# Kernel tuning notes

Hardware: AMD Instinct MI355X
Metric: run time of the kernel (lower is better)

The kernel has to match this reference:

```python
import jax, jax.numpy as jnp
import numpy as np

B, N, D, H = 4, 8192, 1024, 16
HD = D // H  # head dim 64
EPS = 1e-5


def setup_inputs() -> dict:
    key = jax.random.key(0)
    ks = jax.random.split(key, 12)
    s = 1.0 / np.sqrt(D)
    return {
        "query": jax.random.normal(ks[0], (B, N, D), jnp.float32),
        "Wq": jax.random.normal(ks[1], (D, D), jnp.float32) * s,
        "bq": jax.random.normal(ks[2], (D,), jnp.float32) * 0.01,
        "Wk": jax.random.normal(ks[3], (D, D), jnp.float32) * s,
        "bk": jax.random.normal(ks[4], (D,), jnp.float32) * 0.01,
        "Wv": jax.random.normal(ks[5], (D, D), jnp.float32) * s,
        "bv": jax.random.normal(ks[6], (D,), jnp.float32) * 0.01,
        "Wu": jax.random.normal(ks[7], (D, D), jnp.float32) * s,
        "bu": jax.random.normal(ks[8], (D,), jnp.float32) * 0.01,
        "Wo": jax.random.normal(ks[9], (D, D), jnp.float32) * s,
        "bo": jax.random.normal(ks[10], (D,), jnp.float32) * 0.01,
        "ln_w": jnp.ones((D,), jnp.float32),
        "ln_b": jnp.zeros((D,), jnp.float32),
    }


def _abs_clamp(t, min_mag=0.01, max_mag=100.0):
    return jnp.clip(jnp.abs(t), min_mag, max_mag) * jnp.sign(t)


def _heads(x):  # [b, n, h*d] -> [b, h, n, d]
    b, n, _ = x.shape
    return x.reshape(b, n, H, HD).transpose(0, 2, 1, 3)


def reference(query, Wq, bq, Wk, bk, Wv, bv, Wu, bu, Wo, bo, ln_w, ln_b):
    q = jax.nn.relu(_heads(query @ Wq + bq))  # [b,h,n,d]
    k = jax.nn.relu(_heads(query @ Wk + bk))
    v = _heads(query @ Wv + bv)
    u = query @ Wu + bu  # [b,n,D]
    # global linear-attention reduction: kv[b,h,d,e] = sum_n k v
    kv = jnp.einsum('bhnd,bhne->bhde', k, v)
    kv = _abs_clamp(kv)
    out = jnp.einsum('bhnd,bhde->bhne', q, kv)  # [b,h,n,d]
    out = out.transpose(0, 2, 1, 3).reshape(query.shape)  # [b,n,D]
    # LayerNorm over last dim
    mu = jnp.mean(out, axis=-1, keepdims=True)
    var = jnp.var(out, axis=-1, keepdims=True)
    out = (out - mu) * jax.lax.rsqrt(var + EPS) * ln_w + ln_b
    out = u * out
    return out @ Wo + bo
```

## Files before the change

kernel.cpp:

```cpp
#include <hip/hip_runtime.h>

#define M_TOT 32768

typedef float f32x4 __attribute__((ext_vector_type(4)));
typedef short s16x8 __attribute__((ext_vector_type(8)));

#define AS1(p) ((__attribute__((address_space(1))) void*)(p))
#define AS3(p) ((__attribute__((address_space(3))) void*)(p))

#define BARRIER() asm volatile("s_barrier" ::: "memory")
#define VMCNT4() asm volatile("s_waitcnt vmcnt(4)" ::: "memory")
#define VMCNT2() asm volatile("s_waitcnt vmcnt(2)" ::: "memory")
#define VMCNT0() asm volatile("s_waitcnt vmcnt(0)" ::: "memory")

__device__ __forceinline__ short f2bf(float f) {
    unsigned u = __builtin_bit_cast(unsigned, f);
    u += 0x7fffu + ((u >> 16) & 1u);
    return (short)(u >> 16);
}
__device__ __forceinline__ float bf2f(short s) {
    unsigned u = ((unsigned)(unsigned short)s) << 16;
    return __builtin_bit_cast(float, u);
}

__global__ void conv_x(const float* __restrict__ x, short* __restrict__ y) {
    const size_t nchunk = (size_t)M_TOT * 1024 / 8;
    const size_t stride = (size_t)gridDim.x * blockDim.x;
    for (size_t c = (size_t)blockIdx.x * blockDim.x + threadIdx.x; c < nchunk; c += stride) {
        const float4* src = (const float4*)(x + c * 8);
        float4 a = src[0], b = src[1];
        s16x8 r;
        r[0] = f2bf(a.x); r[1] = f2bf(a.y); r[2] = f2bf(a.z); r[3] = f2bf(a.w);
        r[4] = f2bf(b.x); r[5] = f2bf(b.y); r[6] = f2bf(b.z); r[7] = f2bf(b.w);
        *(s16x8*)(y + c * 8) = r;
    }
}

__global__ void conv_w(const float* __restrict__ Wq, const float* __restrict__ Wk,
                       const float* __restrict__ Wv, const float* __restrict__ Wu,
                       const float* __restrict__ Wo, short* __restrict__ Wcat) {
    const int c = blockIdx.x * 256 + threadIdx.x;
    const int np = c >> 8;
    const int k0 = (c & 255) << 2;
    const float* W = (np < 1024) ? Wq : (np < 2048) ? Wk : (np < 3072) ? Wv
                   : (np < 4096) ? Wu : Wo;
    const int n = np & 1023;
    short4 r;
    r.x = f2bf(W[(size_t)(k0 + 0) * 1024 + n]);
    r.y = f2bf(W[(size_t)(k0 + 1) * 1024 + n]);
    r.z = f2bf(W[(size_t)(k0 + 2) * 1024 + n]);
    r.w = f2bf(W[(size_t)(k0 + 3) * 1024 + n]);
    *(short4*)(Wcat + (size_t)np * 1024 + k0) = r;
}

__global__ void conv_bias(const float* __restrict__ bq, const float* __restrict__ bk,
                          const float* __restrict__ bv, const float* __restrict__ bu,
                          const float* __restrict__ bo, float* __restrict__ bcat) {
    const int i = blockIdx.x * 256 + threadIdx.x;
    const float* b = (i < 1024) ? bq : (i < 2048) ? bk : (i < 3072) ? bv
                   : (i < 4096) ? bu : bo;
    bcat[i] = b[i & 1023];
}

template <int MODE>
__global__ __launch_bounds__(512, 2) void gemm8(
        const short* __restrict__ A, const short* __restrict__ W,
        const float* __restrict__ bias,
        short* __restrict__ qb, short* __restrict__ ktb,
        short* __restrict__ vtb, short* __restrict__ ub,
        float* __restrict__ outb) {
    extern __shared__ char lds[];
    const int tid = threadIdx.x;
    const int wave = tid >> 6, lane = tid & 63;
    const int r16 = lane & 15, g = lane >> 4;
    const int moff = (wave >> 2) << 7;
    const int noff = (wave & 3) << 6;

    const int nwg = (MODE == 0) ? 2048 : 512;
    const int NB = (MODE == 0) ? 16 : 4;
    const int bid = blockIdx.x;
    const int swz = (bid & 7) * (nwg >> 3) + (bid >> 3);
    const int mblk = swz / NB, nblk = swz % NB;
    const int row0 = mblk << 8, col0 = nblk << 8;

    const int rswz = r16 & 7;
    const int ck0 = (g ^ rswz) << 4;
    const int ck1 = ((4 + g) ^ rswz) << 4;
    const int rowbA = (moff + r16) << 7;
    const int rowbB = (noff + r16) << 7;

    const char* baseA = (const char*)A + (size_t)(row0 + wave * 8 + (lane >> 3)) * 2048
                        + (((lane & 7) ^ ((lane >> 3) & 7)) << 4);
    const char* baseB = (const char*)W + (size_t)(col0 + wave * 8 + (lane >> 3)) * 2048
                        + (((lane & 7) ^ ((lane >> 3) & 7)) << 4);

#define STG(BASE, J, T, DST)                                                   \
    __builtin_amdgcn_global_load_lds(                                          \
        AS1((BASE) + (size_t)(J) * 131072 + (size_t)(T) * 128),                \
        AS3((DST) + (J) * 8192 + wave * 1024), 16, 0, 0)

#define RDA(V, M, BUFA) {                                                      \
    (V)[0] = *(const s16x8*)((BUFA) + rowbA + (M) * 2048 + ck0);               \
    (V)[1] = *(const s16x8*)((BUFA) + rowbA + (M) * 2048 + ck1); }

#define RDB(V, N, BUFB) {                                                      \
    (V)[0] = *(const s16x8*)((BUFB) + rowbB + (N) * 2048 + ck0);               \
    (V)[1] = *(const s16x8*)((BUFB) + rowbB + (N) * 2048 + ck1); }

#define MF16(P)                                                                \
    _Pragma("unroll") for (int kk = 0; kk < 2; ++kk)                           \
        _Pragma("unroll") for (int n = 0; n < 4; ++n) {                        \
            acc[2*(P)][n]   = __builtin_amdgcn_mfma_f32_16x16x32_bf16(afr[0][kk], bfr[n][kk], acc[2*(P)][n], 0, 0, 0);   \
            acc[2*(P)+1][n] = __builtin_amdgcn_mfma_f32_16x16x32_bf16(afr[1][kk], bfr[n][kk], acc[2*(P)+1][n], 0, 0, 0); \
        }

#define TILE(T, DOSTAGE, TR2, TR4) {                                           \
    char* bA_ = lds + ((T) & 1) * 65536; char* bB_ = bA_ + 32768;              \
    char* sA_ = lds + (((T) + 1) & 1) * 65536; char* sB_ = sA_ + 32768;        \
    s16x8 afr[2][2];                                                           \
    if (DOSTAGE) { STG(baseB, 0, (T) + 1, sB_); STG(baseB, 1, (T) + 1, sB_); } \
    _Pragma("unroll") for (int n = 0; n < 4; ++n) RDB(bfr[n], n, bB_);         \
    RDA(afr[0], 0, bA_); RDA(afr[1], 1, bA_);                                  \
    BARRIER(); __builtin_amdgcn_s_setprio(1); MF16(0);                         \
    __builtin_amdgcn_s_setprio(0); BARRIER();                                  \
    if (DOSTAGE) { STG(baseB, 2, (T) + 1, sB_); STG(baseB, 3, (T) + 1, sB_); } \
    RDA(afr[0], 2, bA_); RDA(afr[1], 3, bA_);                                  \
    BARRIER(); __builtin_amdgcn_s_setprio(1); MF16(1);                         \
    __builtin_amdgcn_s_setprio(0); TR2; BARRIER();                             \
    if (DOSTAGE) { STG(baseA, 0, (T) + 1, sA_); STG(baseA, 2, (T) + 1, sA_); } \
    RDA(afr[0], 4, bA_); RDA(afr[1], 5, bA_);                                  \
    BARRIER(); __builtin_amdgcn_s_setprio(1); MF16(2);                         \
    __builtin_amdgcn_s_setprio(0); BARRIER();                                  \
    if (DOSTAGE) { STG(baseA, 1, (T) + 1, sA_); STG(baseA, 3, (T) + 1, sA_); } \
    RDA(afr[0], 6, bA_); RDA(afr[1], 7, bA_);                                  \
    BARRIER(); __builtin_amdgcn_s_setprio(1); MF16(3);                         \
    __builtin_amdgcn_s_setprio(0); TR4; BARRIER();                             \
}

    f32x4 acc[8][4] = {};
    s16x8 bfr[4][2];

    STG(baseB, 0, 0, lds + 32768); STG(baseB, 1, 0, lds + 32768);
    STG(baseB, 2, 0, lds + 32768); STG(baseB, 3, 0, lds + 32768);
    STG(baseA, 0, 0, lds);         STG(baseA, 2, 0, lds);
    STG(baseA, 1, 0, lds);         STG(baseA, 3, 0, lds);
    VMCNT2();
    BARRIER();

    #pragma unroll 1
    for (int t = 0; t < 15; ++t) TILE(t, true, VMCNT4(), VMCNT2());
    TILE(15, false, VMCNT0(), (void)0);

    const int rj = (lane >> 4) << 2;
    if (MODE == 1) {
        #pragma unroll
        for (int n = 0; n < 4; ++n) {
            const int gn = col0 + noff + n * 16 + r16;
            const float bv = bias[gn];
            #pragma unroll
            for (int m = 0; m < 8; ++m) {
                const int gm0 = row0 + moff + m * 16 + rj;
                #pragma unroll
                for (int j = 0; j < 4; ++j)
                    outb[(size_t)(gm0 + j) * 1024 + gn] = acc[m][n][j] + bv;
            }
        }
    } else {
        const int seg = col0 >> 10;
        if (seg == 0 || seg == 3) {
            short* dst = (seg == 0) ? qb : ub;
            const bool do_relu = (seg == 0);
            #pragma unroll
            for (int n = 0; n < 4; ++n) {
                const int gn = col0 + noff + n * 16 + r16;
                const int f = gn & 1023;
                const float bv = bias[gn];
                #pragma unroll
                for (int m = 0; m < 8; ++m) {
                    const int gm0 = row0 + moff + m * 16 + rj;
                    #pragma unroll
                    for (int j = 0; j < 4; ++j) {
                        float val = acc[m][n][j] + bv;
                        if (do_relu) val = fmaxf(val, 0.0f);
                        dst[(size_t)(gm0 + j) * 1024 + f] = f2bf(val);
                    }
                }
            }
        } else {
            short* dst = (seg == 1) ? ktb : vtb;
            const bool do_relu = (seg == 1);
            #pragma unroll
            for (int n = 0; n < 4; ++n) {
                const int gn = col0 + noff + n * 16 + r16;
                const int hd = gn & 1023;
                const float bv = bias[gn];
                #pragma unroll
                for (int m = 0; m < 8; ++m) {
                    const int gm0 = row0 + moff + m * 16 + rj;
                    const int b = gm0 >> 13;
                    const int ntok = gm0 & 8191;
                    float v0 = acc[m][n][0] + bv, v1 = acc[m][n][1] + bv;
                    float v2 = acc[m][n][2] + bv, v3 = acc[m][n][3] + bv;
                    if (do_relu) {
                        v0 = fmaxf(v0, 0.0f); v1 = fmaxf(v1, 0.0f);
                        v2 = fmaxf(v2, 0.0f); v3 = fmaxf(v3, 0.0f);
                    }
                    short4 pk;
                    pk.x = f2bf(v0); pk.y = f2bf(v1); pk.z = f2bf(v2); pk.w = f2bf(v3);
                    *(short4*)(dst + ((size_t)(b * 1024 + hd)) * 8192 + ntok) = pk;
                }
            }
        }
    }
#undef TILE
#undef MF16
#undef RDB
#undef RDA
#undef STG
}

__global__ __launch_bounds__(256) void kv_partial(const short* __restrict__ ktb,
                                                  const short* __restrict__ vtb,
                                                  float* __restrict__ kvp) {
    __shared__ float red[4][4096];
    const int slice = blockIdx.x;
    const int bh = blockIdx.y;
    const int wave = threadIdx.x >> 6, lane = threadIdx.x & 63;
    const int r16 = lane & 15;
    const short* kb = ktb + (size_t)bh * 64 * 8192;
    const short* vb = vtb + (size_t)bh * 64 * 8192;
    const int n0 = (slice << 10) + (wave << 8);
    f32x4 acc[4][4] = {};
    for (int s = 0; s < 8; ++s) {
        const int nk = n0 + (s << 5) + ((lane >> 4) << 3);
        s16x8 af[4], bf[4];
        #pragma unroll
        for (int m = 0; m < 4; ++m) af[m] = *(const s16x8*)(kb + (size_t)(m * 16 + r16) * 8192 + nk);
        #pragma unroll
        for (int n = 0; n < 4; ++n) bf[n] = *(const s16x8*)(vb + (size_t)(n * 16 + r16) * 8192 + nk);
        #pragma unroll
        for (int m = 0; m < 4; ++m)
            #pragma unroll
            for (int n = 0; n < 4; ++n)
                acc[m][n] = __builtin_amdgcn_mfma_f32_16x16x32_bf16(af[m], bf[n], acc[m][n], 0, 0, 0);
    }
    const int rj = (lane >> 4) << 2;
    #pragma unroll
    for (int m = 0; m < 4; ++m)
        #pragma unroll
        for (int n = 0; n < 4; ++n)
            #pragma unroll
            for (int j = 0; j < 4; ++j)
                red[wave][(m * 16 + rj + j) * 64 + n * 16 + r16] = acc[m][n][j];
    __syncthreads();
    float* dst = kvp + ((size_t)slice * 64 + bh) * 4096;
    const int i0 = threadIdx.x * 16;
    #pragma unroll
    for (int e = 0; e < 16; e += 4) {
        f32x4 a0 = *(const f32x4*)&red[0][i0 + e];
        f32x4 a1 = *(const f32x4*)&red[1][i0 + e];
        f32x4 a2 = *(const f32x4*)&red[2][i0 + e];
        f32x4 a3 = *(const f32x4*)&red[3][i0 + e];
        *(f32x4*)&dst[i0 + e] = (a0 + a1) + (a2 + a3);
    }
}

__global__ void kv_reduce(const float* __restrict__ kvp, short* __restrict__ kvt) {
    const int bh = blockIdx.x;
    for (int i = threadIdx.x; i < 4096; i += 256) {
        float s = 0.0f;
        #pragma unroll
        for (int sl = 0; sl < 8; ++sl)
            s += kvp[((size_t)sl * 64 + bh) * 4096 + i];
        float a = fabsf(s);
        float cmag = fminf(fmaxf(a, 0.01f), 100.0f);
        float r = (s > 0.0f) ? cmag : ((s < 0.0f) ? -cmag : 0.0f);
        const int d = i >> 6, e = i & 63;
        kvt[(size_t)bh * 4096 + e * 64 + d] = f2bf(r);
    }
}

__global__ __launch_bounds__(256) void qkv_ln(const short* __restrict__ qb,
                                              const short* __restrict__ kvt,
                                              const short* __restrict__ ub,
                                              const float* __restrict__ lnw,
                                              const float* __restrict__ lnb,
                                              short* __restrict__ yb) {
    __shared__ short tr[4][1024];
    const int wave = threadIdx.x >> 6, lane = threadIdx.x & 63;
    const int r16 = lane & 15, g = lane >> 4;
    const size_t rowB = (size_t)blockIdx.x * 64 + wave * 16;
    const int bh0 = (int)((rowB >> 13) << 4);
    const short* qrow = qb + (rowB + r16) * 1024 + g * 8;

    float s[4] = {0, 0, 0, 0}, sq[4] = {0, 0, 0, 0};
    for (int h = 0; h < 16; ++h) {
        const short* kvb = kvt + (size_t)(bh0 + h) * 4096 + g * 8;
        f32x4 a4[4] = {};
        #pragma unroll
        for (int kk = 0; kk < 2; ++kk) {
            const s16x8 af = *(const s16x8*)(qrow + h * 64 + kk * 32);
            #pragma unroll
            for (int n = 0; n < 4; ++n) {
                const s16x8 bf = *(const s16x8*)(kvb + (n * 16 + r16) * 64 + kk * 32);
                a4[n] = __builtin_amdgcn_mfma_f32_16x16x32_bf16(af, bf, a4[n], 0, 0, 0);
            }
        }
        #pragma unroll
        for (int n = 0; n < 4; ++n)
            #pragma unroll
            for (int j = 0; j < 4; ++j) {
                const float v = a4[n][j];
                s[j] += v; sq[j] += v * v;
            }
    }
    #pragma unroll
    for (int j = 0; j < 4; ++j) {
        #pragma unroll
        for (int mk = 1; mk < 16; mk <<= 1) {
            s[j] += __shfl_xor(s[j], mk);
            sq[j] += __shfl_xor(sq[j], mk);
        }
    }
    float mu[4], rs[4];
    #pragma unroll
    for (int j = 0; j < 4; ++j) {
        mu[j] = s[j] * (1.0f / 1024.0f);
        const float var = sq[j] * (1.0f / 1024.0f) - mu[j] * mu[j];
        rs[j] = rsqrtf(var + 1e-5f);
    }

    short* trw = &tr[wave][0];
    const int rdr = lane >> 3;
    const int c0 = (lane & 7) * 8;
    for (int h = 0; h < 16; ++h) {
        const short* kvb = kvt + (size_t)(bh0 + h) * 4096 + g * 8;
        f32x4 a4[4] = {};
        #pragma unroll
        for (int kk = 0; kk < 2; ++kk) {
            const s16x8 af = *(const s16x8*)(qrow + h * 64 + kk * 32);
            #pragma unroll
            for (int n = 0; n < 4; ++n) {
                const s16x8 bf = *(const s16x8*)(kvb + (n * 16 + r16) * 64 + kk * 32);
                a4[n] = __builtin_amdgcn_mfma_f32_16x16x32_bf16(af, bf, a4[n], 0, 0, 0);
            }
        }
        #pragma unroll
        for (int n = 0; n < 4; ++n) {
            const float lw = lnw[h * 64 + n * 16 + r16];
            const float lb = lnb[h * 64 + n * 16 + r16];
            #pragma unroll
            for (int j = 0; j < 4; ++j) {
                const float val = (a4[n][j] - mu[j]) * rs[j] * lw + lb;
                trw[(g * 4 + j) * 64 + ((n ^ g) * 16 + r16)] = f2bf(val);
            }
        }
        #pragma unroll
        for (int p = 0; p < 2; ++p) {
            const int r = rdr + p * 8;
            const s16x8 t = *(const s16x8*)&trw[r * 64 + (((c0 >> 4) ^ (r >> 2)) * 16) + (c0 & 15)];
            const s16x8 uu = *(const s16x8*)(ub + (rowB + r) * 1024 + h * 64 + c0);
            s16x8 o;
            #pragma unroll
            for (int e = 0; e < 8; ++e)
                o[e] = f2bf(bf2f(t[e]) * bf2f(uu[e]));
            *(s16x8*)(yb + (rowB + r) * 1024 + h * 64 + c0) = o;
        }
    }
}

extern "C" void kernel_launch(void* const* d_in, const int* in_sizes, int n_in,
                              void* d_out, int out_size, void* d_ws, size_t ws_size,
                              hipStream_t stream) {
    (void)in_sizes; (void)n_in; (void)out_size;
    const float* query = (const float*)d_in[0];
    const float* Wq = (const float*)d_in[1];
    const float* bq = (const float*)d_in[2];
    const float* Wk = (const float*)d_in[3];
    const float* bk = (const float*)d_in[4];
    const float* Wv = (const float*)d_in[5];
    const float* bv = (const float*)d_in[6];
    const float* Wu = (const float*)d_in[7];
    const float* bu = (const float*)d_in[8];
    const float* Wo = (const float*)d_in[9];
    const float* bo = (const float*)d_in[10];
    const float* lnw = (const float*)d_in[11];
    const float* lnb = (const float*)d_in[12];
    float* out = (float*)d_out;
    char* ws = (char*)d_ws;
    if (ws_size < 380129280u) return;

    short* Xb   = (short*)(ws);
    short* Wcat = (short*)(ws + 67108864);
    float* bcat = (float*)(ws + 77594624);
    short* qb   = (short*)(ws + 77615104);
    short* ktb  = (short*)(ws + 144723968);
    short* vtb  = (short*)(ws + 211832832);
    short* ub   = (short*)(ws + 278941696);
    float* kvp  = (float*)(ws + 346050560);
    short* kvt  = (short*)(ws + 379604992);
    short* yb   = Xb;

    hipFuncSetAttribute(reinterpret_cast<const void*>(&gemm8<0>),
                        hipFuncAttributeMaxDynamicSharedMemorySize, 131072);
    hipFuncSetAttribute(reinterpret_cast<const void*>(&gemm8<1>),
                        hipFuncAttributeMaxDynamicSharedMemorySize, 131072);

    conv_x<<<2048, 256, 0, stream>>>(query, Xb);
    conv_w<<<5120, 256, 0, stream>>>(Wq, Wk, Wv, Wu, Wo, Wcat);
    conv_bias<<<20, 256, 0, stream>>>(bq, bk, bv, bu, bo, bcat);
    gemm8<0><<<2048, 512, 131072, stream>>>(Xb, Wcat, bcat, qb, ktb, vtb, ub, nullptr);
    kv_partial<<<dim3(8, 64), 256, 0, stream>>>(ktb, vtb, kvp);
    kv_reduce<<<64, 256, 0, stream>>>(kvp, kvt);
    qkv_ln<<<512, 256, 0, stream>>>(qb, kvt, ub, lnw, lnb, yb);
    gemm8<1><<<512, 512, 131072, stream>>>(yb, Wcat + (size_t)4096 * 1024, bcat + 4096,
                                           nullptr, nullptr, nullptr, nullptr, out);
}
```

Baseline: 557.8 us.

## Halve GEMM barrier phases and transpose weights through shared-memory tiles

The GEMM main loop goes from four barrier-separated MFMA phases per K-tile to two. Each phase now issues all four B or A global-to-LDS stages at once and loads four A fragments before the MFMAs, which cuts synchronisation overhead but raises register pressure and changes when staged data is waited on. The waitcnt values passed at the call sites were not updated, so some A loads may still be in flight when they are read. Separately, the weight-conversion kernel now transposes 64x64 tiles through padded LDS, so its global reads are coalesced float4 loads instead of strided scalar reads.

```diff
diff --git a/kernel.cpp b/kernel.cpp
--- a/kernel.cpp
+++ b/kernel.cpp
@@ -36,21 +36,37 @@
     }
 }
 
-__global__ void conv_w(const float* __restrict__ Wq, const float* __restrict__ Wk,
-                       const float* __restrict__ Wv, const float* __restrict__ Wu,
-                       const float* __restrict__ Wo, short* __restrict__ Wcat) {
-    const int c = blockIdx.x * 256 + threadIdx.x;
-    const int np = c >> 8;
-    const int k0 = (c & 255) << 2;
-    const float* W = (np < 1024) ? Wq : (np < 2048) ? Wk : (np < 3072) ? Wv
-                   : (np < 4096) ? Wu : Wo;
-    const int n = np & 1023;
-    short4 r;
-    r.x = f2bf(W[(size_t)(k0 + 0) * 1024 + n]);
-    r.y = f2bf(W[(size_t)(k0 + 1) * 1024 + n]);
-    r.z = f2bf(W[(size_t)(k0 + 2) * 1024 + n]);
-    r.w = f2bf(W[(size_t)(k0 + 3) * 1024 + n]);
-    *(short4*)(Wcat + (size_t)np * 1024 + k0) = r;
+__global__ __launch_bounds__(256) void conv_w(const float* __restrict__ Wq,
+                                              const float* __restrict__ Wk,
+                                              const float* __restrict__ Wv,
+                                              const float* __restrict__ Wu,
+                                              const float* __restrict__ Wo,
+                                              short* __restrict__ Wcat) {
+    __shared__ float t[64][65];
+    const int b = blockIdx.x;
+    const int mat = b >> 8;
+    const int kt = (b >> 4) & 15, nt = b & 15;
+    const int k0 = kt << 6, n0 = nt << 6;
+    const float* W = (mat == 0) ? Wq : (mat == 1) ? Wk : (mat == 2) ? Wv
+                   : (mat == 3) ? Wu : Wo;
+    const int rr = threadIdx.x >> 4;
+    const int cc = threadIdx.x & 15;
+    #pragma unroll
+    for (int p = 0; p < 4; ++p) {
+        const int row = p * 16 + rr;
+        const float4 v = *(const float4*)(W + (size_t)(k0 + row) * 1024 + n0 + cc * 4);
+        t[row][cc * 4 + 0] = v.x; t[row][cc * 4 + 1] = v.y;
+        t[row][cc * 4 + 2] = v.z; t[row][cc * 4 + 3] = v.w;
+    }
+    __syncthreads();
+    #pragma unroll
+    for (int p = 0; p < 4; ++p) {
+        const int nr = p * 16 + rr;
+        short4 r;
+        r.x = f2bf(t[cc * 4 + 0][nr]); r.y = f2bf(t[cc * 4 + 1][nr]);
+        r.z = f2bf(t[cc * 4 + 2][nr]); r.w = f2bf(t[cc * 4 + 3][nr]);
+        *(short4*)(Wcat + (size_t)(mat * 1024 + n0 + nr) * 1024 + k0 + cc * 4) = r;
+    }
 }
 
 __global__ void conv_bias(const float* __restrict__ bq, const float* __restrict__ bk,
@@ -107,35 +123,32 @@
     (V)[0] = *(const s16x8*)((BUFB) + rowbB + (N) * 2048 + ck0);               \
     (V)[1] = *(const s16x8*)((BUFB) + rowbB + (N) * 2048 + ck1); }
 
-#define MF16(P)                                                                \
+#define MF16(P, A0, A1)                                                        \
     _Pragma("unroll") for (int kk = 0; kk < 2; ++kk)                           \
         _Pragma("unroll") for (int n = 0; n < 4; ++n) {                        \
-            acc[2*(P)][n]   = __builtin_amdgcn_mfma_f32_16x16x32_bf16(afr[0][kk], bfr[n][kk], acc[2*(P)][n], 0, 0, 0);   \
-            acc[2*(P)+1][n] = __builtin_amdgcn_mfma_f32_16x16x32_bf16(afr[1][kk], bfr[n][kk], acc[2*(P)+1][n], 0, 0, 0); \
-        }
-
-#define TILE(T, DOSTAGE, TR2, TR4) {                                           \
+            acc[2*(P)][n]   = __builtin_amdgcn_mfma_f32_16x16x32_bf16((A0)[kk], bfr[n][kk], acc[2*(P)][n], 0, 0, 0);   \
+            acc[2*(P)+1][n] = __builtin_amdgcn_mfma_f32_16x16x32_bf16((A1)[kk], bfr[n][kk], acc[2*(P)+1][n], 0, 0, 0); \
+        }
+
+#define TILE(T, DOSTAGE, TRmid, TRend) {                                       \
     char* bA_ = lds + ((T) & 1) * 65536; char* bB_ = bA_ + 32768;              \
     char* sA_ = lds + (((T) + 1) & 1) * 65536; char* sB_ = sA_ + 32768;        \
-    s16x8 afr[2][2];                                                           \
-    if (DOSTAGE) { STG(baseB, 0, (T) + 1, sB_); STG(baseB, 1, (T) + 1, sB_); } \
+    s16x8 a0[2], a1[2], a2[2], a3[2];                                          \
+    if (DOSTAGE) { STG(baseB, 0, (T) + 1, sB_); STG(baseB, 1, (T) + 1, sB_);   \
+                   STG(baseB, 2, (T) + 1, sB_); STG(baseB, 3, (T) + 1, sB_); } \
     _Pragma("unroll") for (int n = 0; n < 4; ++n) RDB(bfr[n], n, bB_);         \
-    RDA(afr[0], 0, bA_); RDA(afr[1], 1, bA_);                                  \
-    BARRIER(); __builtin_amdgcn_s_setprio(1); MF16(0);                         \
-    __builtin_amdgcn_s_setprio(0); BARRIER();                                  \
-    if (DOSTAGE) { STG(baseB, 2, (T) + 1, sB_); STG(baseB, 3, (T) + 1, sB_); } \
-    RDA(afr[0], 2, bA_); RDA(afr[1], 3, bA_);                                  \
-    BARRIER(); __builtin_amdgcn_s_setprio(1); MF16(1);                         \
-    __builtin_amdgcn_s_setprio(0); TR2; BARRIER();                             \
-    if (DOSTAGE) { STG(baseA, 0, (T) + 1, sA_); STG(baseA, 2, (T) + 1, sA_); } \
-    RDA(afr[0], 4, bA_); RDA(afr[1], 5, bA_);                                  \
-    BARRIER(); __builtin_amdgcn_s_setprio(1); MF16(2);                         \
-    __builtin_amdgcn_s_setprio(0); BARRIER();                                  \
-    if (DOSTAGE) { STG(baseA, 1, (T) + 1, sA_); STG(baseA, 3, (T) + 1, sA_); } \
-    RDA(afr[0], 6, bA_); RDA(afr[1], 7, bA_);                                  \
-    BARRIER(); __builtin_amdgcn_s_setprio(1); MF16(3);                         \
-    __builtin_amdgcn_s_setprio(0); TR4; BARRIER();                             \
-}
+    RDA(a0, 0, bA_); RDA(a1, 1, bA_); RDA(a2, 2, bA_); RDA(a3, 3, bA_);        \
+    __builtin_amdgcn_s_setprio(1);                                             \
+    MF16(0, a0, a1); MF16(1, a2, a3);                                          \
+    __builtin_amdgcn_s_setprio(0);                                             \
+    TRmid; BARRIER();                                                          \
+    if (DOSTAGE) { STG(baseA, 0, (T) + 1, sA_); STG(baseA, 2, (T) + 1, sA_);   \
+                   STG(baseA, 1, (T) + 1, sA_); STG(baseA, 3, (T) + 1, sA_); } \
+    RDA(a0, 4, bA_); RDA(a1, 5, bA_); RDA(a2, 6, bA_); RDA(a3, 7, bA_);        \
+    __builtin_amdgcn_s_setprio(1);                                             \
+    MF16(2, a0, a1); MF16(3, a2, a3);                                          \
+    __builtin_amdgcn_s_setprio(0);                                             \
+    TRend; BARRIER(); }
 
     f32x4 acc[8][4] = {};
     s16x8 bfr[4][2];
@@ -407,7 +420,7 @@
                         hipFuncAttributeMaxDynamicSharedMemorySize, 131072);
 
     conv_x<<<2048, 256, 0, stream>>>(query, Xb);
-    conv_w<<<5120, 256, 0, stream>>>(Wq, Wk, Wv, Wu, Wo, Wcat);
+    conv_w<<<1280, 256, 0, stream>>>(Wq, Wk, Wv, Wu, Wo, Wcat);
     conv_bias<<<20, 256, 0, stream>>>(bq, bk, bv, bu, bo, bcat);
     gemm8<0><<<2048, 512, 131072, stream>>>(Xb, Wcat, bcat, qb, ktb, vtb, ub, nullptr);
     kv_partial<<<dim3(8, 64), 256, 0, stream>>>(ktb, vtb, kvp);
```

Measured after the change: 537.4 us. 3.6% less time.
